# Optimization experiments

Hardware: AMD Instinct MI355X
Metric: run time of the kernel (lower is better)

## Reference

```python
import jax, jax.numpy as jnp
import numpy as np
import math

D_MODEL = 512
N_HEADS = 8
D_K = D_MODEL // N_HEADS
B, S = 2, 4096
LN_EPS = 1e-5


def _xavier(key, fan_in, fan_out):
    limit = math.sqrt(6.0 / (fan_in + fan_out))
    return jax.random.uniform(key, (fan_in, fan_out), jnp.float32, -limit, limit)


def setup_inputs() -> dict:
    key = jax.random.key(0)
    ks = jax.random.split(key, 12)
    x = jax.random.normal(ks[0], (B, S, D_MODEL), jnp.float32)
    consciousness_state = jax.random.normal(ks[1], (B, D_MODEL), jnp.float32)
    # weights stored as [in, out] (equivalent to torch Linear weight.T)
    w_q = _xavier(ks[2], D_MODEL, D_MODEL)
    w_k = _xavier(ks[3], D_MODEL, D_MODEL)
    w_v = _xavier(ks[4], D_MODEL, D_MODEL)
    w_o = _xavier(ks[5], D_MODEL, D_MODEL)
    b_o = jnp.zeros((D_MODEL,), jnp.float32)
    w_gate = _xavier(ks[6], D_MODEL, N_HEADS)
    b_gate = jnp.zeros((N_HEADS,), jnp.float32)
    w_int = _xavier(ks[7], D_MODEL, D_MODEL)
    b_int = jnp.zeros((D_MODEL,), jnp.float32)
    ln_gamma = jnp.ones((D_MODEL,), jnp.float32)
    ln_beta = jnp.zeros((D_MODEL,), jnp.float32)
    return {"x": x, "consciousness_state": consciousness_state,
            "w_q": w_q, "w_k": w_k, "w_v": w_v, "w_o": w_o, "b_o": b_o,
            "w_gate": w_gate, "b_gate": b_gate, "w_int": w_int, "b_int": b_int,
            "ln_gamma": ln_gamma, "ln_beta": ln_beta}


def reference(x, consciousness_state, w_q, w_k, w_v, w_o, b_o,
              w_gate, b_gate, w_int, b_int, ln_gamma, ln_beta):
    b, s, d = x.shape
    # project and split heads: [B, H, S, d_k]
    def heads(w):
        return (x @ w).reshape(b, s, N_HEADS, D_K).transpose(0, 2, 1, 3)
    Q, K, V = heads(w_q), heads(w_k), heads(w_v)
    scores = jnp.einsum('bhsd,bhtd->bhst', Q, K) / math.sqrt(D_K)  # [B,H,S,S]
    # per-head consciousness gate BEFORE softmax
    cw = jax.nn.sigmoid(consciousness_state @ w_gate + b_gate)  # [B,H]
    scores = scores * cw[:, :, None, None]
    attn = jax.nn.softmax(scores, axis=-1)
    # dropout is identity in eval mode
    context = jnp.einsum('bhst,bhtd->bhsd', attn, V)
    context = context.transpose(0, 2, 1, 3).reshape(b, s, d)
    out = context @ w_o + b_o
    iw = jax.nn.sigmoid(consciousness_state @ w_int + b_int)  # [B,D]
    out = out * iw[:, None, :]
    # residual + LayerNorm
    h = out + x
    mu = jnp.mean(h, axis=-1, keepdims=True)
    var = jnp.var(h, axis=-1, keepdims=True)
    out = (h - mu) * jax.lax.rsqrt(var + LN_EPS) * ln_gamma + ln_beta
    return out, attn.mean(axis=1)
```

## Files before the change

### kernel.cpp

```cpp
#include <hip/hip_runtime.h>
#include <hip/hip_bf16.h>

using short8 = __attribute__((ext_vector_type(8))) short;
using f32x4  = __attribute__((ext_vector_type(4))) float;

#define S_LEN 4096
#define DM 512

__device__ __forceinline__ unsigned short f2b(float f) {
    unsigned int u = __float_as_uint(f);
    u += 0x7fffu + ((u >> 16) & 1u);
    return (unsigned short)(u >> 16);
}

__device__ __forceinline__ short8 pack8(float4 a, float4 b) {
    short8 r;
    r[0] = (short)f2b(a.x); r[1] = (short)f2b(a.y); r[2] = (short)f2b(a.z); r[3] = (short)f2b(a.w);
    r[4] = (short)f2b(b.x); r[5] = (short)f2b(b.y); r[6] = (short)f2b(b.z); r[7] = (short)f2b(b.w);
    return r;
}

__global__ __launch_bounds__(256) void convert_w(
    const float* __restrict__ w0, const float* __restrict__ w1,
    const float* __restrict__ w2, const float* __restrict__ w3,
    unsigned short* __restrict__ t0, unsigned short* __restrict__ t1,
    unsigned short* __restrict__ t2, unsigned short* __restrict__ t3)
{
    __shared__ float sh[64][65];
    const float* src; unsigned short* dst;
    switch (blockIdx.z) {
        case 0: src = w0; dst = t0; break;
        case 1: src = w1; dst = t1; break;
        case 2: src = w2; dst = t2; break;
        default: src = w3; dst = t3; break;
    }
    int k0 = blockIdx.x * 64, n0 = blockIdx.y * 64;
    int tid = threadIdx.x;
    for (int i = tid; i < 4096; i += 256) {
        int k = i >> 6, n = i & 63;
        sh[k][n] = src[(size_t)(k0 + k) * DM + n0 + n];
    }
    __syncthreads();
    for (int i = tid; i < 4096; i += 256) {
        int n = i >> 6, k = i & 63;
        dst[(size_t)(n0 + n) * DM + k0 + k] = f2b(sh[k][n]);
    }
}

__global__ __launch_bounds__(256) void convert_x(
    const float* __restrict__ x, unsigned short* __restrict__ xb)
{
    size_t i = ((size_t)blockIdx.x * 256 + threadIdx.x) * 8;
    float4 a = *reinterpret_cast<const float4*>(x + i);
    float4 b = *reinterpret_cast<const float4*>(x + i + 4);
    *reinterpret_cast<short8*>(xb + i) = pack8(a, b);
}

__global__ __launch_bounds__(64) void gates_kernel(
    const float* __restrict__ cs, const float* __restrict__ wg, const float* __restrict__ bg,
    const float* __restrict__ wi, const float* __restrict__ bi,
    float* __restrict__ cwout, float* __restrict__ iwout)
{
    int o = blockIdx.x, b = blockIdx.y, lane = threadIdx.x;
    const float* c = cs + (size_t)b * DM;
    float acc = 0.f;
    if (o < 8) {
        #pragma unroll
        for (int j = 0; j < 8; ++j) { int k = j * 64 + lane; acc += c[k] * wg[(size_t)k * 8 + o]; }
    } else {
        int n = o - 8;
        #pragma unroll
        for (int j = 0; j < 8; ++j) { int k = j * 64 + lane; acc += c[k] * wi[(size_t)k * DM + n]; }
    }
    #pragma unroll
    for (int d = 32; d; d >>= 1) acc += __shfl_xor(acc, d);
    if (lane == 0) {
        if (o < 8) cwout[b * 8 + o] = 1.f / (1.f + __expf(-(acc + bg[o])));
        else       iwout[b * DM + (o - 8)] = 1.f / (1.f + __expf(-(acc + bi[o - 8])));
    }
}

__global__ __launch_bounds__(256) void gemm_qkv(
    const unsigned short* __restrict__ A, const unsigned short* __restrict__ WT,
    unsigned short* __restrict__ Qb, unsigned short* __restrict__ Kb,
    unsigned short* __restrict__ Vt)
{
    __shared__ unsigned short a_sh[64][72];
    __shared__ unsigned short b_sh[64][72];
    const int m0 = blockIdx.x * 64;
    const int n0g = blockIdx.y * 64;
    const int which = blockIdx.y >> 3;
    const int tid = threadIdx.x;
    const int wave = tid >> 6, lane = tid & 63;
    const int g = lane >> 4, lr = lane & 15;
    const int srow = tid >> 3, skc = (tid & 7) * 8;

    f32x4 acc[4];
    #pragma unroll
    for (int i = 0; i < 4; ++i) acc[i] = (f32x4){0.f, 0.f, 0.f, 0.f};

    short8 ar[2], br[2];
    #pragma unroll
    for (int cc = 0; cc < 2; ++cc) {
        int row = srow + cc * 32;
        ar[cc] = *reinterpret_cast<const short8*>(A  + (size_t)(m0  + row) * DM + skc);
        br[cc] = *reinterpret_cast<const short8*>(WT + (size_t)(n0g + row) * DM + skc);
    }

    for (int k0 = 0; k0 < 512; k0 += 64) {
        #pragma unroll
        for (int cc = 0; cc < 2; ++cc) {
            int row = srow + cc * 32;
            *reinterpret_cast<short8*>(&a_sh[row][skc]) = ar[cc];
            *reinterpret_cast<short8*>(&b_sh[row][skc]) = br[cc];
        }
        __syncthreads();
        if (k0 + 64 < 512) {
            #pragma unroll
            for (int cc = 0; cc < 2; ++cc) {
                int row = srow + cc * 32;
                ar[cc] = *reinterpret_cast<const short8*>(A  + (size_t)(m0  + row) * DM + k0 + 64 + skc);
                br[cc] = *reinterpret_cast<const short8*>(WT + (size_t)(n0g + row) * DM + k0 + 64 + skc);
            }
        }
        #pragma unroll
        for (int ks = 0; ks < 2; ++ks) {
            short8 af = *reinterpret_cast<const short8*>(&a_sh[wave * 16 + lr][ks * 32 + g * 8]);
            #pragma unroll
            for (int nf = 0; nf < 4; ++nf) {
                short8 bf = *reinterpret_cast<const short8*>(&b_sh[nf * 16 + lr][ks * 32 + g * 8]);
                acc[nf] = __builtin_amdgcn_mfma_f32_16x16x32_bf16(af, bf, acc[nf], 0, 0, 0);
            }
        }
        __syncthreads();
    }

    #pragma unroll
    for (int nf = 0; nf < 4; ++nf) {
        #pragma unroll
        for (int r = 0; r < 4; ++r) {
            int m = m0 + wave * 16 + g * 4 + r;
            int nl = (blockIdx.y & 7) * 64 + nf * 16 + lr;
            unsigned short v = f2b(acc[nf][r]);
            if (which == 0) {
                Qb[(size_t)m * DM + nl] = v;
            } else if (which == 1) {
                Kb[(size_t)m * DM + nl] = v;
            } else {
                int b = m >> 12, s = m & 4095;
                int h = nl >> 6, d = nl & 63;
                Vt[((size_t)(b * 8 + h) * 64 + d) * S_LEN + s] = v;
            }
        }
    }
}

__global__ __launch_bounds__(256) void gemm_proj(
    const unsigned short* __restrict__ A, const unsigned short* __restrict__ WT,
    float* __restrict__ outf, const float* __restrict__ bias,
    const float* __restrict__ iw, const float* __restrict__ xres)
{
    __shared__ unsigned short a_sh[64][72];
    __shared__ unsigned short b_sh[64][72];
    const int m0 = blockIdx.x * 64;
    const int n0 = blockIdx.y * 64;
    const int tid = threadIdx.x;
    const int wave = tid >> 6, lane = tid & 63;
    const int g = lane >> 4, lr = lane & 15;
    const int srow = tid >> 3, skc = (tid & 7) * 8;

    f32x4 acc[4];
    #pragma unroll
    for (int i = 0; i < 4; ++i) acc[i] = (f32x4){0.f, 0.f, 0.f, 0.f};

    short8 ar[2], br[2];
    #pragma unroll
    for (int cc = 0; cc < 2; ++cc) {
        int row = srow + cc * 32;
        ar[cc] = *reinterpret_cast<const short8*>(A  + (size_t)(m0 + row) * DM + skc);
        br[cc] = *reinterpret_cast<const short8*>(WT + (size_t)(n0 + row) * DM + skc);
    }

    for (int k0 = 0; k0 < 512; k0 += 64) {
        #pragma unroll
        for (int cc = 0; cc < 2; ++cc) {
            int row = srow + cc * 32;
            *reinterpret_cast<short8*>(&a_sh[row][skc]) = ar[cc];
            *reinterpret_cast<short8*>(&b_sh[row][skc]) = br[cc];
        }
        __syncthreads();
        if (k0 + 64 < 512) {
            #pragma unroll
            for (int cc = 0; cc < 2; ++cc) {
                int row = srow + cc * 32;
                ar[cc] = *reinterpret_cast<const short8*>(A  + (size_t)(m0 + row) * DM + k0 + 64 + skc);
                br[cc] = *reinterpret_cast<const short8*>(WT + (size_t)(n0 + row) * DM + k0 + 64 + skc);
            }
        }
        #pragma unroll
        for (int ks = 0; ks < 2; ++ks) {
            short8 af = *reinterpret_cast<const short8*>(&a_sh[wave * 16 + lr][ks * 32 + g * 8]);
            #pragma unroll
            for (int nf = 0; nf < 4; ++nf) {
                short8 bf = *reinterpret_cast<const short8*>(&b_sh[nf * 16 + lr][ks * 32 + g * 8]);
                acc[nf] = __builtin_amdgcn_mfma_f32_16x16x32_bf16(af, bf, acc[nf], 0, 0, 0);
            }
        }
        __syncthreads();
    }

    #pragma unroll
    for (int nf = 0; nf < 4; ++nf) {
        #pragma unroll
        for (int r = 0; r < 4; ++r) {
            int m = m0 + wave * 16 + g * 4 + r;
            int n = n0 + nf * 16 + lr;
            int b = m >> 12;
            float v = (acc[nf][r] + bias[n]) * iw[b * DM + n] + xres[(size_t)m * DM + n];
            outf[(size_t)m * DM + n] = v;
        }
    }
}

__global__ __launch_bounds__(256) void attn_ctx(
    const unsigned short* __restrict__ Qb, const unsigned short* __restrict__ Kb,
    const unsigned short* __restrict__ Vt, const float* __restrict__ cw,
    float* __restrict__ lbuf, unsigned short* __restrict__ ctx)
{
    __shared__ unsigned short k_sh[64][72];
    __shared__ unsigned short v_sh[64][72];
    __shared__ unsigned short p_sh[4][16][72];
    const int q0 = blockIdx.x * 64;
    const int bh = blockIdx.y;
    const int b = bh >> 3, h = bh & 7;
    const int tid = threadIdx.x, wave = tid >> 6, lane = tid & 63;
    const int g = lane >> 4, lr = lane & 15;
    const int srow = tid >> 3, skc = (tid & 7) * 8;

    const float sc2 = cw[bh] * 0.125f * 1.44269504f;
    short8 qf[2];
    {
        const unsigned short* qp = Qb + (size_t)(b * S_LEN + q0 + wave * 16 + lr) * DM + h * 64;
        qf[0] = *reinterpret_cast<const short8*>(qp + g * 8);
        qf[1] = *reinterpret_cast<const short8*>(qp + 32 + g * 8);
    }
    float lacc = 0.f;
    f32x4 cacc[4];
    #pragma unroll
    for (int i = 0; i < 4; ++i) cacc[i] = (f32x4){0.f, 0.f, 0.f, 0.f};

    const unsigned short* Kbase = Kb + (size_t)(b * S_LEN) * DM + h * 64;
    const unsigned short* Vbase = Vt + ((size_t)bh * 64) * S_LEN;

    short8 kr[2], vr[2];
    #pragma unroll
    for (int cc = 0; cc < 2; ++cc) {
        int row = srow + cc * 32;
        kr[cc] = *reinterpret_cast<const short8*>(Kbase + (size_t)row * DM + skc);
        vr[cc] = *reinterpret_cast<const short8*>(Vbase + (size_t)row * S_LEN + skc);
    }

    for (int kv0 = 0; kv0 < S_LEN; kv0 += 64) {
        #pragma unroll
        for (int cc = 0; cc < 2; ++cc) {
            int row = srow + cc * 32;
            *reinterpret_cast<short8*>(&k_sh[row][skc]) = kr[cc];
            *reinterpret_cast<short8*>(&v_sh[row][skc]) = vr[cc];
        }
        __syncthreads();
        f32x4 st[4];
        #pragma unroll
        for (int f = 0; f < 4; ++f) st[f] = (f32x4){0.f, 0.f, 0.f, 0.f};
        #pragma unroll
        for (int ks = 0; ks < 2; ++ks) {
            #pragma unroll
            for (int f = 0; f < 4; ++f) {
                short8 kf = *reinterpret_cast<const short8*>(&k_sh[f * 16 + lr][ks * 32 + g * 8]);
                st[f] = __builtin_amdgcn_mfma_f32_16x16x32_bf16(kf, qf[ks], st[f], 0, 0, 0);
            }
        }
        if (kv0 + 64 < S_LEN) {
            #pragma unroll
            for (int cc = 0; cc < 2; ++cc) {
                int row = srow + cc * 32;
                kr[cc] = *reinterpret_cast<const short8*>(Kbase + (size_t)(kv0 + 64 + row) * DM + skc);
                vr[cc] = *reinterpret_cast<const short8*>(Vbase + (size_t)row * S_LEN + kv0 + 64 + skc);
            }
        }
        #pragma unroll
        for (int f = 0; f < 4; ++f) {
            float p0 = __builtin_amdgcn_exp2f(st[f][0] * sc2);
            float p1 = __builtin_amdgcn_exp2f(st[f][1] * sc2);
            float p2 = __builtin_amdgcn_exp2f(st[f][2] * sc2);
            float p3 = __builtin_amdgcn_exp2f(st[f][3] * sc2);
            lacc += (p0 + p1) + (p2 + p3);
            unsigned u0, u1;
            asm("v_cvt_pk_bf16_f32 %0, %1, %2" : "=v"(u0) : "v"(p0), "v"(p1));
            asm("v_cvt_pk_bf16_f32 %0, %1, %2" : "=v"(u1) : "v"(p2), "v"(p3));
            uint2 pv; pv.x = u0; pv.y = u1;
            *reinterpret_cast<uint2*>(&p_sh[wave][lr][f * 16 + g * 4]) = pv;
        }
        #pragma unroll
        for (int ks = 0; ks < 2; ++ks) {
            short8 pf = *reinterpret_cast<const short8*>(&p_sh[wave][lr][ks * 32 + g * 8]);
            #pragma unroll
            for (int df = 0; df < 4; ++df) {
                short8 vf = *reinterpret_cast<const short8*>(&v_sh[df * 16 + lr][ks * 32 + g * 8]);
                cacc[df] = __builtin_amdgcn_mfma_f32_16x16x32_bf16(pf, vf, cacc[df], 0, 0, 0);
            }
        }
        __syncthreads();
    }
    float l = lacc;
    l += __shfl_xor(l, 16);
    l += __shfl_xor(l, 32);
    float rl = 1.f / l;
    if (lane < 16) lbuf[bh * S_LEN + q0 + wave * 16 + lr] = l;
    float rlv[4];
    #pragma unroll
    for (int r = 0; r < 4; ++r) rlv[r] = __shfl(rl, g * 4 + r);
    #pragma unroll
    for (int df = 0; df < 4; ++df) {
        #pragma unroll
        for (int r = 0; r < 4; ++r) {
            int q = q0 + wave * 16 + g * 4 + r;
            ctx[(size_t)(b * S_LEN + q) * DM + h * 64 + df * 16 + lr] = f2b(cacc[df][r] * rlv[r]);
        }
    }
}

__global__ __launch_bounds__(256) void attn_mean(
    const unsigned short* __restrict__ Qb, const unsigned short* __restrict__ Kb,
    const float* __restrict__ cw, const float* __restrict__ lbuf,
    float* __restrict__ outmean)
{
    __shared__ unsigned short k_sh[32][520];
    const int kc0 = blockIdx.x * 512;
    const int q0 = blockIdx.y * 64;
    const int b = blockIdx.z;
    const int tid = threadIdx.x, wave = tid >> 6, lane = tid & 63;
    const int g = lane >> 4, lr = lane & 15;
    const int srow = tid >> 6, scol = (tid & 63) * 8;

    float la2[8][4], sc2[8];
    #pragma unroll
    for (int h = 0; h < 8; ++h) {
        sc2[h] = cw[b * 8 + h] * 0.125f * 1.44269504f;
        #pragma unroll
        for (int r = 0; r < 4; ++r) {
            int idx = (b * 8 + h) * S_LEN + q0 + wave * 16 + g * 4 + r;
            la2[h][r] = -log2f(lbuf[idx]);
        }
    }
    const unsigned short* qbase = Qb + (size_t)(b * S_LEN + q0 + wave * 16 + lr) * DM;
    const unsigned short* Kbase = Kb + (size_t)(b * S_LEN) * DM;

    short8 stg[8];
    #pragma unroll
    for (int i = 0; i < 8; ++i) {
        int row = srow + i * 4;
        stg[i] = *reinterpret_cast<const short8*>(Kbase + (size_t)(kc0 + row) * DM + scol);
    }

    for (int t = 0; t < 16; ++t) {
        int kv0 = kc0 + t * 32;
        #pragma unroll
        for (int i = 0; i < 8; ++i) {
            int row = srow + i * 4;
            *reinterpret_cast<short8*>(&k_sh[row][scol]) = stg[i];
        }
        __syncthreads();
        if (t + 1 < 16) {
            #pragma unroll
            for (int i = 0; i < 8; ++i) {
                int row = srow + i * 4;
                stg[i] = *reinterpret_cast<const short8*>(Kbase + (size_t)(kv0 + 32 + row) * DM + scol);
            }
        }
        float macc[2][4];
        #pragma unroll
        for (int f = 0; f < 2; ++f)
            #pragma unroll
            for (int r = 0; r < 4; ++r) macc[f][r] = 0.f;
        #pragma unroll
        for (int h = 0; h < 8; ++h) {
            const unsigned short* qp = qbase + h * 64;
            short8 qf0 = *reinterpret_cast<const short8*>(qp + g * 8);
            short8 qf1 = *reinterpret_cast<const short8*>(qp + 32 + g * 8);
            f32x4 s[2];
            s[0] = (f32x4){0.f, 0.f, 0.f, 0.f};
            s[1] = (f32x4){0.f, 0.f, 0.f, 0.f};
            #pragma unroll
            for (int f = 0; f < 2; ++f) {
                short8 kf0 = *reinterpret_cast<const short8*>(&k_sh[f * 16 + lr][h * 64 + g * 8]);
                s[f] = __builtin_amdgcn_mfma_f32_16x16x32_bf16(qf0, kf0, s[f], 0, 0, 0);
                short8 kf1 = *reinterpret_cast<const short8*>(&k_sh[f * 16 + lr][h * 64 + 32 + g * 8]);
                s[f] = __builtin_amdgcn_mfma_f32_16x16x32_bf16(qf1, kf1, s[f], 0, 0, 0);
            }
            #pragma unroll
            for (int f = 0; f < 2; ++f)
                #pragma unroll
                for (int r = 0; r < 4; ++r)
                    macc[f][r] += __builtin_amdgcn_exp2f(s[f][r] * sc2[h] + la2[h][r]);
        }
        #pragma unroll
        for (int f = 0; f < 2; ++f) {
            #pragma unroll
            for (int r = 0; r < 4; ++r) {
                int q = q0 + wave * 16 + g * 4 + r;
                outmean[(size_t)(b * S_LEN + q) * S_LEN + kv0 + f * 16 + lr] = macc[f][r] * 0.125f;
            }
        }
        __syncthreads();
    }
}

__global__ __launch_bounds__(64) void ln_kernel(
    const float* __restrict__ hbuf, const float* __restrict__ gamma,
    const float* __restrict__ beta, float* __restrict__ dout)
{
    int row = blockIdx.x, lane = threadIdx.x;
    const float* hp = hbuf + (size_t)row * DM + lane * 8;
    float4 v0 = *reinterpret_cast<const float4*>(hp);
    float4 v1 = *reinterpret_cast<const float4*>(hp + 4);
    float s = v0.x + v0.y + v0.z + v0.w + v1.x + v1.y + v1.z + v1.w;
    float ss = v0.x * v0.x + v0.y * v0.y + v0.z * v0.z + v0.w * v0.w
             + v1.x * v1.x + v1.y * v1.y + v1.z * v1.z + v1.w * v1.w;
    #pragma unroll
    for (int d = 32; d; d >>= 1) { s += __shfl_xor(s, d); ss += __shfl_xor(ss, d); }
    float mu = s * (1.f / 512.f);
    float var = ss * (1.f / 512.f) - mu * mu;
    float rstd = rsqrtf(var + 1e-5f);
    float4 g0 = *reinterpret_cast<const float4*>(gamma + lane * 8);
    float4 g1 = *reinterpret_cast<const float4*>(gamma + lane * 8 + 4);
    float4 b0 = *reinterpret_cast<const float4*>(beta + lane * 8);
    float4 b1 = *reinterpret_cast<const float4*>(beta + lane * 8 + 4);
    float4 o0, o1;
    o0.x = (v0.x - mu) * rstd * g0.x + b0.x;
    o0.y = (v0.y - mu) * rstd * g0.y + b0.y;
    o0.z = (v0.z - mu) * rstd * g0.z + b0.z;
    o0.w = (v0.w - mu) * rstd * g0.w + b0.w;
    o1.x = (v1.x - mu) * rstd * g1.x + b1.x;
    o1.y = (v1.y - mu) * rstd * g1.y + b1.y;
    o1.z = (v1.z - mu) * rstd * g1.z + b1.z;
    o1.w = (v1.w - mu) * rstd * g1.w + b1.w;
    float* op = dout + (size_t)row * DM + lane * 8;
    *reinterpret_cast<float4*>(op) = o0;
    *reinterpret_cast<float4*>(op + 4) = o1;
}

extern "C" void kernel_launch(void* const* d_in, const int* in_sizes, int n_in,
                              void* d_out, int out_size, void* d_ws, size_t ws_size,
                              hipStream_t stream)
{
    const float* x   = (const float*)d_in[0];
    const float* cs  = (const float*)d_in[1];
    const float* wq  = (const float*)d_in[2];
    const float* wk  = (const float*)d_in[3];
    const float* wv  = (const float*)d_in[4];
    const float* wo  = (const float*)d_in[5];
    const float* bo  = (const float*)d_in[6];
    const float* wg  = (const float*)d_in[7];
    const float* bg  = (const float*)d_in[8];
    const float* wi  = (const float*)d_in[9];
    const float* bi  = (const float*)d_in[10];
    const float* gam = (const float*)d_in[11];
    const float* bet = (const float*)d_in[12];

    float* out = (float*)d_out;
    float* outmean = out + (size_t)2 * S_LEN * DM;

    char* ws = (char*)d_ws;
    size_t off = 0;
    auto alloc = [&](size_t bytes) { void* p = ws + off; off += (bytes + 255) & ~(size_t)255; return p; };

    unsigned short* wtq = (unsigned short*)alloc((size_t)DM * DM * 2);
    unsigned short* wtk = (unsigned short*)alloc((size_t)DM * DM * 2);
    unsigned short* wtv = (unsigned short*)alloc((size_t)DM * DM * 2);
    unsigned short* wto = (unsigned short*)alloc((size_t)DM * DM * 2);
    unsigned short* xb  = (unsigned short*)alloc((size_t)2 * S_LEN * DM * 2);
    unsigned short* Qb  = (unsigned short*)alloc((size_t)2 * S_LEN * DM * 2);
    unsigned short* Kb  = (unsigned short*)alloc((size_t)2 * S_LEN * DM * 2);
    unsigned short* Vt  = (unsigned short*)alloc((size_t)2 * S_LEN * DM * 2);
    unsigned short* ctx = (unsigned short*)alloc((size_t)2 * S_LEN * DM * 2);
    float* lbuf = (float*)alloc((size_t)16 * S_LEN * 4);
    float* cwb  = (float*)alloc(64);
    float* iwb  = (float*)alloc((size_t)2 * DM * 4);
    float* hbuf = (float*)Qb;

    convert_w<<<dim3(8, 8, 4), 256, 0, stream>>>(wq, wk, wv, wo, wtq, wtk, wtv, wto);
    convert_x<<<dim3(2048), 256, 0, stream>>>(x, xb);
    gates_kernel<<<dim3(520, 2), 64, 0, stream>>>(cs, wg, bg, wi, bi, cwb, iwb);

    gemm_qkv<<<dim3(128, 24), 256, 0, stream>>>(xb, wtq, Qb, Kb, Vt);

    attn_ctx<<<dim3(64, 16), 256, 0, stream>>>(Qb, Kb, Vt, cwb, lbuf, ctx);
    attn_mean<<<dim3(8, 64, 2), 256, 0, stream>>>(Qb, Kb, cwb, lbuf, outmean);

    gemm_proj<<<dim3(128, 8), 256, 0, stream>>>(ctx, wto, hbuf, bo, iwb, x);
    ln_kernel<<<dim3(2 * S_LEN), 64, 0, stream>>>(hbuf, gam, bet, out);
}
```

Before: 282.2 us.

## Fold softmax scale into Q projection and compute row sums via MFMA

Multiplies the per-head gate, 1/sqrt(dk) and log2(e) into Q when it is written in the QKV GEMM epilogue, so the attention kernels no longer multiply every score by a scale. The softmax denominator is now accumulated with an extra MFMA against a vector of bf16 ones instead of scalar adds followed by shuffles. The 1/8 head mean is folded into the log offset. s_setprio hints are wrapped around the MFMA sections of the GEMM and attention kernels. The cost is an extra rounding, because the scaled Q is stored in bf16 and the row sums are taken from bf16-rounded probabilities.

```diff
diff --git a/kernel.cpp b/kernel.cpp
--- a/kernel.cpp
+++ b/kernel.cpp
@@ -82,6 +82,7 @@
 
 __global__ __launch_bounds__(256) void gemm_qkv(
     const unsigned short* __restrict__ A, const unsigned short* __restrict__ WT,
+    const float* __restrict__ cw,
     unsigned short* __restrict__ Qb, unsigned short* __restrict__ Kb,
     unsigned short* __restrict__ Vt)
 {
@@ -95,6 +96,13 @@
     const int g = lane >> 4, lr = lane & 15;
     const int srow = tid >> 3, skc = (tid & 7) * 8;
 
+    float sq = 1.f;
+    if (which == 0) {
+        int b = blockIdx.x >> 6;
+        int h = blockIdx.y & 7;
+        sq = cw[b * 8 + h] * 0.125f * 1.44269504f;
+    }
+
     f32x4 acc[4];
     #pragma unroll
     for (int i = 0; i < 4; ++i) acc[i] = (f32x4){0.f, 0.f, 0.f, 0.f};
@@ -123,6 +131,7 @@
                 br[cc] = *reinterpret_cast<const short8*>(WT + (size_t)(n0g + row) * DM + k0 + 64 + skc);
             }
         }
+        __builtin_amdgcn_s_setprio(1);
         #pragma unroll
         for (int ks = 0; ks < 2; ++ks) {
             short8 af = *reinterpret_cast<const short8*>(&a_sh[wave * 16 + lr][ks * 32 + g * 8]);
@@ -132,6 +141,7 @@
                 acc[nf] = __builtin_amdgcn_mfma_f32_16x16x32_bf16(af, bf, acc[nf], 0, 0, 0);
             }
         }
+        __builtin_amdgcn_s_setprio(0);
         __syncthreads();
     }
 
@@ -141,7 +151,7 @@
         for (int r = 0; r < 4; ++r) {
             int m = m0 + wave * 16 + g * 4 + r;
             int nl = (blockIdx.y & 7) * 64 + nf * 16 + lr;
-            unsigned short v = f2b(acc[nf][r]);
+            unsigned short v = f2b(acc[nf][r] * sq);
             if (which == 0) {
                 Qb[(size_t)m * DM + nl] = v;
             } else if (which == 1) {
@@ -197,6 +207,7 @@
                 br[cc] = *reinterpret_cast<const short8*>(WT + (size_t)(n0 + row) * DM + k0 + 64 + skc);
             }
         }
+        __builtin_amdgcn_s_setprio(1);
         #pragma unroll
         for (int ks = 0; ks < 2; ++ks) {
             short8 af = *reinterpret_cast<const short8*>(&a_sh[wave * 16 + lr][ks * 32 + g * 8]);
@@ -206,6 +217,7 @@
                 acc[nf] = __builtin_amdgcn_mfma_f32_16x16x32_bf16(af, bf, acc[nf], 0, 0, 0);
             }
         }
+        __builtin_amdgcn_s_setprio(0);
         __syncthreads();
     }
 
@@ -224,7 +236,7 @@
 
 __global__ __launch_bounds__(256) void attn_ctx(
     const unsigned short* __restrict__ Qb, const unsigned short* __restrict__ Kb,
-    const unsigned short* __restrict__ Vt, const float* __restrict__ cw,
+    const unsigned short* __restrict__ Vt,
     float* __restrict__ lbuf, unsigned short* __restrict__ ctx)
 {
     __shared__ unsigned short k_sh[64][72];
@@ -237,14 +249,17 @@
     const int g = lane >> 4, lr = lane & 15;
     const int srow = tid >> 3, skc = (tid & 7) * 8;
 
-    const float sc2 = cw[bh] * 0.125f * 1.44269504f;
     short8 qf[2];
     {
         const unsigned short* qp = Qb + (size_t)(b * S_LEN + q0 + wave * 16 + lr) * DM + h * 64;
         qf[0] = *reinterpret_cast<const short8*>(qp + g * 8);
         qf[1] = *reinterpret_cast<const short8*>(qp + 32 + g * 8);
     }
-    float lacc = 0.f;
+    short8 onesb;
+    #pragma unroll
+    for (int i = 0; i < 8; ++i) onesb[i] = (short)0x3F80;
+
+    f32x4 lsum = (f32x4){0.f, 0.f, 0.f, 0.f};
     f32x4 cacc[4];
     #pragma unroll
     for (int i = 0; i < 4; ++i) cacc[i] = (f32x4){0.f, 0.f, 0.f, 0.f};
@@ -271,6 +286,7 @@
         f32x4 st[4];
         #pragma unroll
         for (int f = 0; f < 4; ++f) st[f] = (f32x4){0.f, 0.f, 0.f, 0.f};
+        __builtin_amdgcn_s_setprio(1);
         #pragma unroll
         for (int ks = 0; ks < 2; ++ks) {
             #pragma unroll
@@ -279,6 +295,7 @@
                 st[f] = __builtin_amdgcn_mfma_f32_16x16x32_bf16(kf, qf[ks], st[f], 0, 0, 0);
             }
         }
+        __builtin_amdgcn_s_setprio(0);
         if (kv0 + 64 < S_LEN) {
             #pragma unroll
             for (int cc = 0; cc < 2; ++cc) {
@@ -289,50 +306,51 @@
         }
         #pragma unroll
         for (int f = 0; f < 4; ++f) {
-            float p0 = __builtin_amdgcn_exp2f(st[f][0] * sc2);
-            float p1 = __builtin_amdgcn_exp2f(st[f][1] * sc2);
-            float p2 = __builtin_amdgcn_exp2f(st[f][2] * sc2);
-            float p3 = __builtin_amdgcn_exp2f(st[f][3] * sc2);
-            lacc += (p0 + p1) + (p2 + p3);
+            float p0 = __builtin_amdgcn_exp2f(st[f][0]);
+            float p1 = __builtin_amdgcn_exp2f(st[f][1]);
+            float p2 = __builtin_amdgcn_exp2f(st[f][2]);
+            float p3 = __builtin_amdgcn_exp2f(st[f][3]);
             unsigned u0, u1;
             asm("v_cvt_pk_bf16_f32 %0, %1, %2" : "=v"(u0) : "v"(p0), "v"(p1));
             asm("v_cvt_pk_bf16_f32 %0, %1, %2" : "=v"(u1) : "v"(p2), "v"(p3));
             uint2 pv; pv.x = u0; pv.y = u1;
             *reinterpret_cast<uint2*>(&p_sh[wave][lr][f * 16 + g * 4]) = pv;
         }
+        __builtin_amdgcn_s_setprio(1);
         #pragma unroll
         for (int ks = 0; ks < 2; ++ks) {
             short8 pf = *reinterpret_cast<const short8*>(&p_sh[wave][lr][ks * 32 + g * 8]);
+            lsum = __builtin_amdgcn_mfma_f32_16x16x32_bf16(pf, onesb, lsum, 0, 0, 0);
             #pragma unroll
             for (int df = 0; df < 4; ++df) {
                 short8 vf = *reinterpret_cast<const short8*>(&v_sh[df * 16 + lr][ks * 32 + g * 8]);
                 cacc[df] = __builtin_amdgcn_mfma_f32_16x16x32_bf16(pf, vf, cacc[df], 0, 0, 0);
             }
         }
-        __syncthreads();
-    }
-    float l = lacc;
-    l += __shfl_xor(l, 16);
-    l += __shfl_xor(l, 32);
-    float rl = 1.f / l;
-    if (lane < 16) lbuf[bh * S_LEN + q0 + wave * 16 + lr] = l;
-    float rlv[4];
-    #pragma unroll
-    for (int r = 0; r < 4; ++r) rlv[r] = __shfl(rl, g * 4 + r);
+        __builtin_amdgcn_s_setprio(0);
+        __syncthreads();
+    }
+    float rl[4];
+    #pragma unroll
+    for (int r = 0; r < 4; ++r) rl[r] = 1.f / lsum[r];
+    if (lr == 0) {
+        #pragma unroll
+        for (int r = 0; r < 4; ++r)
+            lbuf[bh * S_LEN + q0 + wave * 16 + g * 4 + r] = lsum[r];
+    }
     #pragma unroll
     for (int df = 0; df < 4; ++df) {
         #pragma unroll
         for (int r = 0; r < 4; ++r) {
             int q = q0 + wave * 16 + g * 4 + r;
-            ctx[(size_t)(b * S_LEN + q) * DM + h * 64 + df * 16 + lr] = f2b(cacc[df][r] * rlv[r]);
+            ctx[(size_t)(b * S_LEN + q) * DM + h * 64 + df * 16 + lr] = f2b(cacc[df][r] * rl[r]);
         }
     }
 }
 
 __global__ __launch_bounds__(256) void attn_mean(
     const unsigned short* __restrict__ Qb, const unsigned short* __restrict__ Kb,
-    const float* __restrict__ cw, const float* __restrict__ lbuf,
-    float* __restrict__ outmean)
+    const float* __restrict__ lbuf, float* __restrict__ outmean)
 {
     __shared__ unsigned short k_sh[32][520];
     const int kc0 = blockIdx.x * 512;
@@ -342,14 +360,13 @@
     const int g = lane >> 4, lr = lane & 15;
     const int srow = tid >> 6, scol = (tid & 63) * 8;
 
-    float la2[8][4], sc2[8];
+    float la2[8][4];
     #pragma unroll
     for (int h = 0; h < 8; ++h) {
-        sc2[h] = cw[b * 8 + h] * 0.125f * 1.44269504f;
         #pragma unroll
         for (int r = 0; r < 4; ++r) {
             int idx = (b * 8 + h) * S_LEN + q0 + wave * 16 + g * 4 + r;
-            la2[h][r] = -log2f(lbuf[idx]);
+            la2[h][r] = -log2f(lbuf[idx]) - 3.0f;
         }
     }
     const unsigned short* qbase = Qb + (size_t)(b * S_LEN + q0 + wave * 16 + lr) * DM;
@@ -390,6 +407,7 @@
             f32x4 s[2];
             s[0] = (f32x4){0.f, 0.f, 0.f, 0.f};
             s[1] = (f32x4){0.f, 0.f, 0.f, 0.f};
+            __builtin_amdgcn_s_setprio(1);
             #pragma unroll
             for (int f = 0; f < 2; ++f) {
                 short8 kf0 = *reinterpret_cast<const short8*>(&k_sh[f * 16 + lr][h * 64 + g * 8]);
@@ -397,18 +415,19 @@
                 short8 kf1 = *reinterpret_cast<const short8*>(&k_sh[f * 16 + lr][h * 64 + 32 + g * 8]);
                 s[f] = __builtin_amdgcn_mfma_f32_16x16x32_bf16(qf1, kf1, s[f], 0, 0, 0);
             }
+            __builtin_amdgcn_s_setprio(0);
             #pragma unroll
             for (int f = 0; f < 2; ++f)
                 #pragma unroll
                 for (int r = 0; r < 4; ++r)
-                    macc[f][r] += __builtin_amdgcn_exp2f(s[f][r] * sc2[h] + la2[h][r]);
+                    macc[f][r] += __builtin_amdgcn_exp2f(s[f][r] + la2[h][r]);
         }
         #pragma unroll
         for (int f = 0; f < 2; ++f) {
             #pragma unroll
             for (int r = 0; r < 4; ++r) {
                 int q = q0 + wave * 16 + g * 4 + r;
-                outmean[(size_t)(b * S_LEN + q) * S_LEN + kv0 + f * 16 + lr] = macc[f][r] * 0.125f;
+                outmean[(size_t)(b * S_LEN + q) * S_LEN + kv0 + f * 16 + lr] = macc[f][r];
             }
         }
         __syncthreads();
@@ -492,10 +511,10 @@
     convert_x<<<dim3(2048), 256, 0, stream>>>(x, xb);
     gates_kernel<<<dim3(520, 2), 64, 0, stream>>>(cs, wg, bg, wi, bi, cwb, iwb);
 
-    gemm_qkv<<<dim3(128, 24), 256, 0, stream>>>(xb, wtq, Qb, Kb, Vt);
-
-    attn_ctx<<<dim3(64, 16), 256, 0, stream>>>(Qb, Kb, Vt, cwb, lbuf, ctx);
-    attn_mean<<<dim3(8, 64, 2), 256, 0, stream>>>(Qb, Kb, cwb, lbuf, outmean);
+    gemm_qkv<<<dim3(128, 24), 256, 0, stream>>>(xb, wtq, cwb, Qb, Kb, Vt);
+
+    attn_ctx<<<dim3(64, 16), 256, 0, stream>>>(Qb, Kb, Vt, lbuf, ctx);
+    attn_mean<<<dim3(8, 64, 2), 256, 0, stream>>>(Qb, Kb, lbuf, outmean);
 
     gemm_proj<<<dim3(128, 8), 256, 0, stream>>>(ctx, wto, hbuf, bo, iwb, x);
     ln_kernel<<<dim3(2 * S_LEN), 64, 0, stream>>>(hbuf, gam, bet, out);
```

After: 277.4 us. About the same (-1.7%).
